# Performance work log

Measured on AMD Instinct MI355X. Metric: run time of the kernel, lower is better.

## Reference

```python
import jax, jax.numpy as jnp
import numpy as np

ROPE_BASE = 10000.0


def _rope(x):
    # x: (B, S, H, D) -- rotate-half RoPE applied per head over the sequence dim
    B, S, H, D = x.shape
    half = D // 2
    inv_freq = 1.0 / (ROPE_BASE ** (jnp.arange(half, dtype=jnp.float32) / half))
    ang = jnp.arange(S, dtype=jnp.float32)[:, None] * inv_freq[None, :]  # (S, half)
    cos = jnp.cos(ang)[None, :, None, :].astype(x.dtype)
    sin = jnp.sin(ang)[None, :, None, :].astype(x.dtype)
    x1, x2 = x[..., :half], x[..., half:]
    return jnp.concatenate([x1 * cos - x2 * sin, x2 * cos + x1 * sin], axis=-1)


def setup_inputs() -> dict:
    key = jax.random.key(0)
    ks = jax.random.split(key, 7)
    B, S, D = 8, 1024, 512
    HD = 512  # num_heads * key_dim = 8 * 64
    scale = 0.02
    return {
        "query": jax.random.normal(ks[0], (B, S, D), dtype=jnp.float32),
        "value": jax.random.normal(ks[1], (B, S, D), dtype=jnp.float32),
        "key_in": jax.random.normal(ks[2], (B, S, D), dtype=jnp.float32),
        "Wq": jax.random.normal(ks[3], (D, HD), dtype=jnp.float32) * scale,
        "Wk": jax.random.normal(ks[4], (D, HD), dtype=jnp.float32) * scale,
        "Wv": jax.random.normal(ks[5], (D, HD), dtype=jnp.float32) * scale,
        "Wo": jax.random.normal(ks[6], (HD, D), dtype=jnp.float32) * scale,
    }


def reference(query, value, key_in, Wq, Wk, Wv, Wo):
    H, Dh = 8, 64
    B, Sq, _ = query.shape
    Sk = key_in.shape[1]
    # QKV projections, split heads: (B, S, H, Dh)
    q = (query @ Wq).reshape(B, Sq, H, Dh)
    v = (value @ Wv).reshape(B, Sk, H, Dh)
    k = (key_in @ Wk).reshape(B, Sk, H, Dh)
    # inline RoPE on q and k (applied before head transpose, as in the original)
    q = _rope(q)
    k = _rope(k)
    # scaled dot-product attention with causal mask
    q = q * (1.0 / jnp.sqrt(jnp.asarray(Dh, q.dtype)))
    scores = jnp.einsum("bqhd,bkhd->bhqk", q, k)  # (B, H, Sq, Sk)
    causal = jnp.tril(jnp.ones((Sq, Sk), dtype=bool))[None, None]
    scores = jnp.where(causal, scores, jnp.asarray(-1e9, scores.dtype))
    probs = jax.nn.softmax(scores, axis=-1)
    out = jnp.einsum("bhqk,bkhd->bqhd", probs, v)  # (B, Sq, H, Dh)
    out = out.reshape(B, Sq, H * Dh) @ Wo  # output projection
    return out
```

## Files before the change

### kernel.cpp

```cpp
#include <hip/hip_runtime.h>
#include <hip/hip_bf16.h>
#include <stdint.h>

#define DEV static __device__ __forceinline__

typedef __attribute__((ext_vector_type(8)))  short    s16x8;
typedef __attribute__((ext_vector_type(4)))  short    s16x4;
typedef __attribute__((ext_vector_type(8)))  __bf16   bf16x8;
typedef __attribute__((ext_vector_type(4)))  float    f32x4;
typedef __attribute__((ext_vector_type(16))) float    f32x16;
typedef __attribute__((ext_vector_type(2)))  unsigned u32x2;
typedef __attribute__((ext_vector_type(4)))  unsigned u32x4;

DEV short f2b(float f){
  union{float f; uint32_t i;} x; x.f = f;
  uint32_t r = x.i + 0x7FFFu + ((x.i >> 16) & 1u);
  return (short)(r >> 16);
}
DEV bf16x8 as_bf(s16x8 v){ return __builtin_bit_cast(bf16x8, v); }
DEV float fexp2(float x){ return __builtin_amdgcn_exp2f(x); }
DEV f32x4 mf(s16x8 a, s16x8 b, f32x4 c){
  return __builtin_amdgcn_mfma_f32_16x16x32_bf16(as_bf(a), as_bf(b), c, 0, 0, 0);
}
DEV f32x16 mf32(s16x8 a, s16x8 b, f32x16 c){
  return __builtin_amdgcn_mfma_f32_32x32x16_bf16(as_bf(a), as_bf(b), c, 0, 0, 0);
}

DEV void gload_lds16(const void* g, void* l){
  __builtin_amdgcn_global_load_lds((const __attribute__((address_space(1))) void*)g,
                                   (__attribute__((address_space(3))) void*)l, 16, 0, 0);
}

#if __has_builtin(__builtin_amdgcn_permlane32_swap)
DEV void pswap2(unsigned a, unsigned b, unsigned& x, unsigned& y){
  u32x2 rr = __builtin_amdgcn_permlane32_swap(a, b, false, false);
  x = rr[0]; y = rr[1];
}
DEV float partner32(float v, int hi){
  unsigned u = __builtin_bit_cast(unsigned, v);
  u32x2 rr = __builtin_amdgcn_permlane32_swap(u, u, false, false);
  return __builtin_bit_cast(float, hi ? rr[0] : rr[1]);
}
#else
DEV void pswap2(unsigned a, unsigned b, unsigned& x, unsigned& y){
  unsigned pa_ = (unsigned)__shfl_xor((int)a, 32, 64);
  unsigned pb_ = (unsigned)__shfl_xor((int)b, 32, 64);
  int lo = ((threadIdx.x & 63) < 32);
  x = lo ? a   : pb_;
  y = lo ? pa_ : b;
}
DEV float partner32(float v, int hi){ (void)hi; return __shfl_xor(v, 32, 64); }
#endif

__global__ __launch_bounds__(256) void k_conv3(const float* __restrict__ q,
                                               const float* __restrict__ k,
                                               const float* __restrict__ v,
                                               short* __restrict__ out){
  int z = blockIdx.z;
  const float* in = (z == 0) ? q : (z == 1) ? k : v;
  int i = (blockIdx.x * 256 + threadIdx.x) * 4;
  float4 val = *(const float4*)(in + i);
  short o[4] = { f2b(val.x), f2b(val.y), f2b(val.z), f2b(val.w) };
  *(uint2*)(out + (size_t)z * 4194304 + i) = *(uint2*)o;
}

__global__ __launch_bounds__(256) void k_wt4(const float* __restrict__ w0,
                                             const float* __restrict__ w1,
                                             const float* __restrict__ w2,
                                             const float* __restrict__ w3,
                                             short* __restrict__ wt){
  __shared__ float tile[32][33];
  int z = blockIdx.z;
  const float* w = (z == 0) ? w0 : (z == 1) ? w1 : (z == 2) ? w2 : w3;
  short* o = wt + (size_t)z * 262144;
  int bx = blockIdx.x * 32, by = blockIdx.y * 32;
  int tx = threadIdx.x, ty = threadIdx.y;
  for (int j = 0; j < 32; j += 8)
    tile[ty + j][tx] = w[(size_t)(by + ty + j) * 512 + bx + tx];
  __syncthreads();
  for (int j = 0; j < 32; j += 8)
    o[(size_t)(bx + ty + j) * 512 + by + tx] = f2b(tile[tx][ty + j]);
}

__global__ __launch_bounds__(256) void k_table(float* __restrict__ tab){
  int idx = blockIdx.x * 256 + threadIdx.x;
  int s = idx >> 5, j = idx & 31;
  float inv = __expf(-(float)j * (1.0f / 32.0f) * logf(10000.0f));
  float ang = (float)s * inv;
  tab[idx * 2 + 0] = cosf(ang);
  tab[idx * 2 + 1] = sinf(ang);
}

__global__ __launch_bounds__(256) void k_qkv(const short* __restrict__ Xq,
                                             const short* __restrict__ Xk,
                                             const short* __restrict__ Xv,
                                             const short* __restrict__ Wcat,
                                             const float* __restrict__ tab,
                                             short* __restrict__ Qa,
                                             short* __restrict__ Ka,
                                             short* __restrict__ Vt){
  __shared__ __align__(16) short Al[128 * 32];
  __shared__ __align__(16) short Bl[128 * 32];
  const int t = threadIdx.x;
  const int w = t >> 6, lane = t & 63, fr = lane & 15, fg = lane >> 4;
  const int sel = blockIdx.y >> 2;
  const short* X = (sel == 0) ? Xq : (sel == 1) ? Xk : Xv;
  const int bm = blockIdx.x * 128, bn = blockIdx.y * 128;
  const int wm = (w >> 1) * 64, wn = (w & 1) * 64;
  const int r8 = t >> 2, c8 = (t & 3) * 8;
  f32x4 acc[4][4] = {};
  for (int k0 = 0; k0 < 512; k0 += 32){
    __syncthreads();
#pragma unroll
    for (int j = 0; j < 2; j++){
      const short* ga = X    + (size_t)(bm + j * 64 + r8) * 512 + (k0 + c8);
      const short* gb = Wcat + (size_t)(bn + j * 64 + r8) * 512 + (k0 + c8);
      gload_lds16(ga, &Al[j * 2048 + w * 512]);
      gload_lds16(gb, &Bl[j * 2048 + w * 512]);
    }
    __syncthreads();
    s16x8 af[4], bv[4];
#pragma unroll
    for (int f = 0; f < 4; f++){
      af[f] = *(const s16x8*)(&Al[(wm + f * 16 + fr) * 32 + fg * 8]);
      bv[f] = *(const s16x8*)(&Bl[(wn + f * 16 + fr) * 32 + fg * 8]);
    }
#pragma unroll
    for (int i = 0; i < 4; i++)
#pragma unroll
      for (int jj = 0; jj < 4; jj++)
        acc[i][jj] = __builtin_amdgcn_mfma_f32_16x16x32_bf16(as_bf(af[i]), as_bf(bv[jj]),
                                                             acc[i][jj], 0, 0, 0);
  }
  const int row0 = bm + wm + fg * 4;
  const int b = row0 >> 10;
  const int s_base = row0 & 1023;
  const int hh = (((blockIdx.y & 3) * 128) + wn) >> 6;
  if (sel < 2){
    const float scale = (sel == 0) ? 0.125f * 1.44269504f : 1.0f;
    short* out = (sel == 0) ? Qa : Ka;
#pragma unroll
    for (int i = 0; i < 4; i++)
#pragma unroll
      for (int jj = 0; jj < 2; jj++){
        int d = jj * 16 + fr;
#pragma unroll
        for (int r = 0; r < 4; r++){
          int s = s_base + i * 16 + r;
          float2 cs = *(const float2*)(tab + (size_t)(s * 32 + d) * 2);
          float x1 = acc[i][jj][r], x2 = acc[i][jj + 2][r];
          size_t ob = ((size_t)((b * 8 + hh) * 1024 + s)) * 64 + d;
          out[ob]      = f2b((x1 * cs.x - x2 * cs.y) * scale);
          out[ob + 32] = f2b((x2 * cs.x + x1 * cs.y) * scale);
        }
      }
  } else {
#pragma unroll
    for (int i = 0; i < 4; i++)
#pragma unroll
      for (int jj = 0; jj < 4; jj++){
        int d = jj * 16 + fr;
        s16x4 pk;
#pragma unroll
        for (int r = 0; r < 4; r++) pk[r] = f2b(acc[i][jj][r]);
        size_t ob = ((size_t)((b * 8 + hh) * 64 + d)) * 1024 + s_base + i * 16;
        *(s16x4*)(Vt + ob) = pk;
      }
  }
}

__global__ __launch_bounds__(128) void k_attn(const short* __restrict__ Qb,
                                              const short* __restrict__ Kb,
                                              const short* __restrict__ Vt,
                                              short* __restrict__ O){
  __shared__ __align__(16) short KL[2][4096];
  __shared__ __align__(16) short VL[2][4096];
  const int bid = blockIdx.x;
  const int podr[16] = {15,14,13,12, 0,1,2,3, 11,10,9,8, 4,5,6,7};
  const int Bi = podr[bid >> 6];
  const int bh = bid & 63;
  const int B0 = Bi * 64;
  const int t = threadIdx.x, w = t >> 6, lane = t & 63;
  const int col = lane & 31, hi = lane >> 5;
  const short* Qp = Qb + (size_t)bh * 65536;
  const short* Kp = Kb + (size_t)bh * 65536;
  const short* Vp = Vt + (size_t)bh * 65536;
  const int qrow = B0 + 2 * col + w;

  s16x8 qb[4];
#pragma unroll
  for (int ks = 0; ks < 4; ks++)
    qb[ks] = *(const s16x8*)(Qp + (size_t)qrow * 64 + ks * 16 + hi * 8);

  int crow[16];
#pragma unroll
  for (int r = 0; r < 16; r++) crow[r] = (r & 3) + 8 * (r >> 2) + 4 * hi;

  f32x16 oacc[2] = {};
  float m = -1e30f, l = 0.f;

  auto stage = [&](int buf, int kv0){
#pragma unroll
    for (int R = 0; R < 4; R++){
      int lin = R * 128 + w * 64 + lane;
      int row = lin >> 3, slot = lin & 7;
      int gs = ((slot ^ (row & 7)) * 8);
      gload_lds16(Kp + (size_t)(kv0 + row) * 64 + gs, &KL[buf][(R * 128 + w * 64) * 8]);
      gload_lds16(Vp + (size_t)row * 1024 + kv0 + gs, &VL[buf][(R * 128 + w * 64) * 8]);
    }
  };

  stage(0, 0);
  __syncthreads();

  int cur = 0;
  for (int kv0 = 0; kv0 <= B0; kv0 += 64){
    if (kv0 < B0) stage(cur ^ 1, kv0 + 64);
    f32x16 sc[2];
#pragma unroll
    for (int f = 0; f < 2; f++){
      f32x16 s = {};
      int row = f * 32 + col, rx = row & 7;
#pragma unroll
      for (int ks = 0; ks < 4; ks++){
        s16x8 ka = *(const s16x8*)(&KL[cur][row * 64 + ((ks * 2 + hi) ^ rx) * 8]);
        s = mf32(ka, qb[ks], s);
      }
      sc[f] = s;
    }
    if (kv0 == B0){
#pragma unroll
      for (int f = 0; f < 2; f++)
#pragma unroll
        for (int r = 0; r < 16; r++){
          int kv = kv0 + f * 32 + crow[r];
          if (kv > qrow) sc[f][r] = -1e30f;
        }
    }
    float tm = -1e30f;
#pragma unroll
    for (int f = 0; f < 2; f++)
#pragma unroll
      for (int r = 0; r < 16; r++) tm = fmaxf(tm, sc[f][r]);
    tm = fmaxf(tm, partner32(tm, hi));
    if (!__all(tm <= m + 8.f)){
      float mn = fmaxf(m, tm);
      float corr = fexp2(m - mn);
      m = mn;
      l *= corr;
      float cpv[16];
#pragma unroll
      for (int r = 0; r < 16; r++) cpv[r] = __shfl(corr, crow[r], 64);
#pragma unroll
      for (int r = 0; r < 16; r++){ oacc[0][r] *= cpv[r]; oacc[1][r] *= cpv[r]; }
    }
    float rs = 0.f;
    unsigned wq[2][8];
#pragma unroll
    for (int f = 0; f < 2; f++)
#pragma unroll
      for (int i = 0; i < 8; i++){
        float p0 = fexp2(sc[f][2 * i]     - m);
        float p1 = fexp2(sc[f][2 * i + 1] - m);
        rs += p0 + p1;
        wq[f][i] = (unsigned)(uint16_t)f2b(p0) | ((unsigned)(uint16_t)f2b(p1) << 16);
      }
    rs += partner32(rs, hi);
    l += rs;
    s16x8 pa[4];
#pragma unroll
    for (int f = 0; f < 2; f++)
#pragma unroll
      for (int half = 0; half < 2; half++){
        unsigned w0, w1, w2, w3;
        pswap2(wq[f][half * 4 + 0], wq[f][half * 4 + 2], w0, w2);
        pswap2(wq[f][half * 4 + 1], wq[f][half * 4 + 3], w1, w3);
        u32x4 uv = { w0, w1, w2, w3 };
        pa[f * 2 + half] = __builtin_bit_cast(s16x8, uv);
      }
#pragma unroll
    for (int ks = 0; ks < 4; ks++)
#pragma unroll
      for (int df = 0; df < 2; df++){
        int row = df * 32 + col;
        s16x8 vb = *(const s16x8*)(&VL[cur][row * 64 + ((ks * 2 + hi) ^ (row & 7)) * 8]);
        oacc[df] = mf32(pa[ks], vb, oacc[df]);
      }
    if (kv0 < B0) __syncthreads();
    cur ^= 1;
  }

  const int b = bh >> 3, h = bh & 7;
  float lf[16];
#pragma unroll
  for (int r = 0; r < 16; r++) lf[r] = __shfl(l, crow[r], 64);
#pragma unroll
  for (int r = 0; r < 16; r++){
    int qq = B0 + 2 * crow[r] + w;
    float inv = 1.0f / lf[r];
    O[(size_t)(b * 1024 + qq) * 512 + h * 64 + col]      = f2b(oacc[0][r] * inv);
    O[(size_t)(b * 1024 + qq) * 512 + h * 64 + 32 + col] = f2b(oacc[1][r] * inv);
  }
}

__global__ __launch_bounds__(256) void k_gemm_out(const short* __restrict__ X,
                                                  const short* __restrict__ Wt,
                                                  float* __restrict__ C){
  __shared__ __align__(16) short Al[128 * 32];
  __shared__ __align__(16) short Bl[128 * 32];
  const int t = threadIdx.x;
  const int w = t >> 6, lane = t & 63, fr = lane & 15, fg = lane >> 4;
  const int bm = blockIdx.x * 128, bn = blockIdx.y * 128;
  const int wm = (w >> 1) * 64, wn = (w & 1) * 64;
  const int r8 = t >> 2, c8 = (t & 3) * 8;
  f32x4 acc[4][4] = {};
  for (int k0 = 0; k0 < 512; k0 += 32){
    __syncthreads();
#pragma unroll
    for (int j = 0; j < 2; j++){
      const short* ga = X  + (size_t)(bm + j * 64 + r8) * 512 + (k0 + c8);
      const short* gb = Wt + (size_t)(bn + j * 64 + r8) * 512 + (k0 + c8);
      gload_lds16(ga, &Al[j * 2048 + w * 512]);
      gload_lds16(gb, &Bl[j * 2048 + w * 512]);
    }
    __syncthreads();
    s16x8 af[4], bv[4];
#pragma unroll
    for (int f = 0; f < 4; f++){
      af[f] = *(const s16x8*)(&Al[(wm + f * 16 + fr) * 32 + fg * 8]);
      bv[f] = *(const s16x8*)(&Bl[(wn + f * 16 + fr) * 32 + fg * 8]);
    }
#pragma unroll
    for (int i = 0; i < 4; i++)
#pragma unroll
      for (int jj = 0; jj < 4; jj++)
        acc[i][jj] = __builtin_amdgcn_mfma_f32_16x16x32_bf16(as_bf(af[i]), as_bf(bv[jj]),
                                                             acc[i][jj], 0, 0, 0);
  }
  const int row0 = bm + wm + fg * 4;
  const int col0 = bn + wn + fr;
#pragma unroll
  for (int i = 0; i < 4; i++)
#pragma unroll
    for (int jj = 0; jj < 4; jj++)
#pragma unroll
      for (int r = 0; r < 4; r++)
        C[(size_t)(row0 + i * 16 + r) * 512 + col0 + jj * 16] = acc[i][jj][r];
}

extern "C" void kernel_launch(void* const* d_in, const int* in_sizes, int n_in,
                              void* d_out, int out_size, void* d_ws, size_t ws_size,
                              hipStream_t stream){
  const float* query  = (const float*)d_in[0];
  const float* value  = (const float*)d_in[1];
  const float* key_in = (const float*)d_in[2];
  const float* Wq     = (const float*)d_in[3];
  const float* Wk     = (const float*)d_in[4];
  const float* Wv     = (const float*)d_in[5];
  const float* Wo     = (const float*)d_in[6];

  char* ws = (char*)d_ws;
  const size_t MB = 1ull << 20;
  short* Xq   = (short*)(ws);
  short* Xk   = (short*)(ws + 8 * MB);
  short* Xv   = (short*)(ws + 16 * MB);
  short* Wcat = (short*)(ws + 24 * MB);
  float* tab  = (float*)(ws + 26 * MB);
  short* Qa   = (short*)(ws + 26 * MB + 256 * 1024);
  short* Ka   = (short*)((char*)Qa + 8 * MB);
  short* Va   = (short*)((char*)Ka + 8 * MB);
  short* Oa   = Xq;
  short* Wot  = Wcat + 786432;

  k_conv3<<<dim3(4096, 1, 3), 256, 0, stream>>>(query, key_in, value, Xq);
  k_wt4<<<dim3(16, 16, 4), dim3(32, 8), 0, stream>>>(Wq, Wk, Wv, Wo, Wcat);
  k_table<<<128, 256, 0, stream>>>(tab);

  k_qkv<<<dim3(64, 12), 256, 0, stream>>>(Xq, Xk, Xv, Wcat, tab, Qa, Ka, Va);

  k_attn<<<1024, 128, 0, stream>>>(Qa, Ka, Va, Oa);

  k_gemm_out<<<dim3(64, 4), 256, 0, stream>>>(Oa, Wot, (float*)d_out);
}
```

Measured before the change: 95.63 us.

## Fuse fp32-to-bf16 activation conversion into QKV GEMM and double-buffer GEMM tiles

Removes the separate conversion kernel: the QKV GEMM now reads fp32 activations directly, converts them to bf16 in registers and writes them to LDS. Both the QKV and output-projection GEMMs get double-buffered LDS tiles, so the next k-slice loads while the current one is being multiplied, with one barrier per iteration. This drops a full read-and-write pass over 48MB of activations and a kernel launch. In exchange, the fp32 A tile is read through registers rather than async LDS loads, and LDS use per block doubles. Because each activation tile is reused across 4 column blocks, the fp32 data is re-read and re-converted once per column block.

```diff
diff --git a/kernel.cpp b/kernel.cpp
--- a/kernel.cpp
+++ b/kernel.cpp
@@ -51,18 +51,6 @@
 }
 DEV float partner32(float v, int hi){ (void)hi; return __shfl_xor(v, 32, 64); }
 #endif
-
-__global__ __launch_bounds__(256) void k_conv3(const float* __restrict__ q,
-                                               const float* __restrict__ k,
-                                               const float* __restrict__ v,
-                                               short* __restrict__ out){
-  int z = blockIdx.z;
-  const float* in = (z == 0) ? q : (z == 1) ? k : v;
-  int i = (blockIdx.x * 256 + threadIdx.x) * 4;
-  float4 val = *(const float4*)(in + i);
-  short o[4] = { f2b(val.x), f2b(val.y), f2b(val.z), f2b(val.w) };
-  *(uint2*)(out + (size_t)z * 4194304 + i) = *(uint2*)o;
-}
 
 __global__ __launch_bounds__(256) void k_wt4(const float* __restrict__ w0,
                                              const float* __restrict__ w1,
@@ -91,47 +79,71 @@
   tab[idx * 2 + 1] = sinf(ang);
 }
 
-__global__ __launch_bounds__(256) void k_qkv(const short* __restrict__ Xq,
-                                             const short* __restrict__ Xk,
-                                             const short* __restrict__ Xv,
+__global__ __launch_bounds__(256) void k_qkv(const float* __restrict__ Xq,
+                                             const float* __restrict__ Xk,
+                                             const float* __restrict__ Xv,
                                              const short* __restrict__ Wcat,
                                              const float* __restrict__ tab,
                                              short* __restrict__ Qa,
                                              short* __restrict__ Ka,
                                              short* __restrict__ Vt){
-  __shared__ __align__(16) short Al[128 * 32];
-  __shared__ __align__(16) short Bl[128 * 32];
+  __shared__ __align__(16) short Al[2][128 * 32];
+  __shared__ __align__(16) short Bl[2][128 * 32];
   const int t = threadIdx.x;
   const int w = t >> 6, lane = t & 63, fr = lane & 15, fg = lane >> 4;
   const int sel = blockIdx.y >> 2;
-  const short* X = (sel == 0) ? Xq : (sel == 1) ? Xk : Xv;
+  const float* X = (sel == 0) ? Xq : (sel == 1) ? Xk : Xv;
   const int bm = blockIdx.x * 128, bn = blockIdx.y * 128;
   const int wm = (w >> 1) * 64, wn = (w & 1) * 64;
   const int r8 = t >> 2, c8 = (t & 3) * 8;
+
+  float4 ua[4];
+  auto ldA = [&](int k0){
+    const float* s0 = X + (size_t)(bm + (t >> 2)) * 512 + k0 + c8;
+    const float* s1 = s0 + 64 * 512;
+    ua[0] = *(const float4*)(s0);
+    ua[1] = *(const float4*)(s0 + 4);
+    ua[2] = *(const float4*)(s1);
+    ua[3] = *(const float4*)(s1 + 4);
+  };
+  auto wrA = [&](int buf){
+    s16x8 p0 = { f2b(ua[0].x), f2b(ua[0].y), f2b(ua[0].z), f2b(ua[0].w),
+                 f2b(ua[1].x), f2b(ua[1].y), f2b(ua[1].z), f2b(ua[1].w) };
+    s16x8 p1 = { f2b(ua[2].x), f2b(ua[2].y), f2b(ua[2].z), f2b(ua[2].w),
+                 f2b(ua[3].x), f2b(ua[3].y), f2b(ua[3].z), f2b(ua[3].w) };
+    *(s16x8*)(&Al[buf][(t >> 2) * 32 + c8])        = p0;
+    *(s16x8*)(&Al[buf][(64 + (t >> 2)) * 32 + c8]) = p1;
+  };
+  auto stB = [&](int buf, int k0){
+#pragma unroll
+    for (int j = 0; j < 2; j++)
+      gload_lds16(Wcat + (size_t)(bn + j * 64 + r8) * 512 + k0 + c8,
+                  &Bl[buf][j * 2048 + w * 512]);
+  };
+
   f32x4 acc[4][4] = {};
-  for (int k0 = 0; k0 < 512; k0 += 32){
+  ldA(0); stB(0, 0); wrA(0);
+  __syncthreads();
+  int cur = 0;
+  for (int t16 = 0; t16 < 16; ++t16){
+    const int k0n = (t16 + 1) * 32;
+    if (t16 < 15){ ldA(k0n); stB(cur ^ 1, k0n); }
+    s16x8 af[4], bv[4];
+#pragma unroll
+    for (int f = 0; f < 4; f++){
+      af[f] = *(const s16x8*)(&Al[cur][(wm + f * 16 + fr) * 32 + fg * 8]);
+      bv[f] = *(const s16x8*)(&Bl[cur][(wn + f * 16 + fr) * 32 + fg * 8]);
+    }
+#pragma unroll
+    for (int i = 0; i < 4; i++)
+#pragma unroll
+      for (int jj = 0; jj < 4; jj++)
+        acc[i][jj] = mf(af[i], bv[jj], acc[i][jj]);
+    if (t16 < 15) wrA(cur ^ 1);
     __syncthreads();
-#pragma unroll
-    for (int j = 0; j < 2; j++){
-      const short* ga = X    + (size_t)(bm + j * 64 + r8) * 512 + (k0 + c8);
-      const short* gb = Wcat + (size_t)(bn + j * 64 + r8) * 512 + (k0 + c8);
-      gload_lds16(ga, &Al[j * 2048 + w * 512]);
-      gload_lds16(gb, &Bl[j * 2048 + w * 512]);
-    }
-    __syncthreads();
-    s16x8 af[4], bv[4];
-#pragma unroll
-    for (int f = 0; f < 4; f++){
-      af[f] = *(const s16x8*)(&Al[(wm + f * 16 + fr) * 32 + fg * 8]);
-      bv[f] = *(const s16x8*)(&Bl[(wn + f * 16 + fr) * 32 + fg * 8]);
-    }
-#pragma unroll
-    for (int i = 0; i < 4; i++)
-#pragma unroll
-      for (int jj = 0; jj < 4; jj++)
-        acc[i][jj] = __builtin_amdgcn_mfma_f32_16x16x32_bf16(as_bf(af[i]), as_bf(bv[jj]),
-                                                             acc[i][jj], 0, 0, 0);
-  }
+    cur ^= 1;
+  }
+
   const int row0 = bm + wm + fg * 4;
   const int b = row0 >> 10;
   const int s_base = row0 & 1023;
@@ -306,36 +318,41 @@
 __global__ __launch_bounds__(256) void k_gemm_out(const short* __restrict__ X,
                                                   const short* __restrict__ Wt,
                                                   float* __restrict__ C){
-  __shared__ __align__(16) short Al[128 * 32];
-  __shared__ __align__(16) short Bl[128 * 32];
+  __shared__ __align__(16) short Al[2][128 * 32];
+  __shared__ __align__(16) short Bl[2][128 * 32];
   const int t = threadIdx.x;
   const int w = t >> 6, lane = t & 63, fr = lane & 15, fg = lane >> 4;
   const int bm = blockIdx.x * 128, bn = blockIdx.y * 128;
   const int wm = (w >> 1) * 64, wn = (w & 1) * 64;
   const int r8 = t >> 2, c8 = (t & 3) * 8;
+
+  auto stage = [&](int buf, int k0){
+#pragma unroll
+    for (int j = 0; j < 2; j++){
+      gload_lds16(X  + (size_t)(bm + j * 64 + r8) * 512 + k0 + c8, &Al[buf][j * 2048 + w * 512]);
+      gload_lds16(Wt + (size_t)(bn + j * 64 + r8) * 512 + k0 + c8, &Bl[buf][j * 2048 + w * 512]);
+    }
+  };
+
   f32x4 acc[4][4] = {};
-  for (int k0 = 0; k0 < 512; k0 += 32){
+  stage(0, 0);
+  __syncthreads();
+  int cur = 0;
+  for (int t16 = 0; t16 < 16; ++t16){
+    if (t16 < 15) stage(cur ^ 1, (t16 + 1) * 32);
+    s16x8 af[4], bv[4];
+#pragma unroll
+    for (int f = 0; f < 4; f++){
+      af[f] = *(const s16x8*)(&Al[cur][(wm + f * 16 + fr) * 32 + fg * 8]);
+      bv[f] = *(const s16x8*)(&Bl[cur][(wn + f * 16 + fr) * 32 + fg * 8]);
+    }
+#pragma unroll
+    for (int i = 0; i < 4; i++)
+#pragma unroll
+      for (int jj = 0; jj < 4; jj++)
+        acc[i][jj] = mf(af[i], bv[jj], acc[i][jj]);
     __syncthreads();
-#pragma unroll
-    for (int j = 0; j < 2; j++){
-      const short* ga = X  + (size_t)(bm + j * 64 + r8) * 512 + (k0 + c8);
-      const short* gb = Wt + (size_t)(bn + j * 64 + r8) * 512 + (k0 + c8);
-      gload_lds16(ga, &Al[j * 2048 + w * 512]);
-      gload_lds16(gb, &Bl[j * 2048 + w * 512]);
-    }
-    __syncthreads();
-    s16x8 af[4], bv[4];
-#pragma unroll
-    for (int f = 0; f < 4; f++){
-      af[f] = *(const s16x8*)(&Al[(wm + f * 16 + fr) * 32 + fg * 8]);
-      bv[f] = *(const s16x8*)(&Bl[(wn + f * 16 + fr) * 32 + fg * 8]);
-    }
-#pragma unroll
-    for (int i = 0; i < 4; i++)
-#pragma unroll
-      for (int jj = 0; jj < 4; jj++)
-        acc[i][jj] = __builtin_amdgcn_mfma_f32_16x16x32_bf16(as_bf(af[i]), as_bf(bv[jj]),
-                                                             acc[i][jj], 0, 0, 0);
+    cur ^= 1;
   }
   const int row0 = bm + wm + fg * 4;
   const int col0 = bn + wn + fr;
@@ -361,22 +378,18 @@
 
   char* ws = (char*)d_ws;
   const size_t MB = 1ull << 20;
-  short* Xq   = (short*)(ws);
-  short* Xk   = (short*)(ws + 8 * MB);
-  short* Xv   = (short*)(ws + 16 * MB);
+  short* Oa   = (short*)(ws);
   short* Wcat = (short*)(ws + 24 * MB);
   float* tab  = (float*)(ws + 26 * MB);
   short* Qa   = (short*)(ws + 26 * MB + 256 * 1024);
   short* Ka   = (short*)((char*)Qa + 8 * MB);
   short* Va   = (short*)((char*)Ka + 8 * MB);
-  short* Oa   = Xq;
   short* Wot  = Wcat + 786432;
 
-  k_conv3<<<dim3(4096, 1, 3), 256, 0, stream>>>(query, key_in, value, Xq);
   k_wt4<<<dim3(16, 16, 4), dim3(32, 8), 0, stream>>>(Wq, Wk, Wv, Wo, Wcat);
   k_table<<<128, 256, 0, stream>>>(tab);
 
-  k_qkv<<<dim3(64, 12), 256, 0, stream>>>(Xq, Xk, Xv, Wcat, tab, Qa, Ka, Va);
+  k_qkv<<<dim3(64, 12), 256, 0, stream>>>(query, key_in, value, Wcat, tab, Qa, Ka, Va);
 
   k_attn<<<1024, 128, 0, stream>>>(Qa, Ka, Va, Oa);
 
```

Measured after the change: 78.78 us. 17.6% less time.
